# Kernel tuning notes

Measured on AMD Instinct MI355X. Metric: run time of the kernel, lower is better.

## Reference

```python
import jax, jax.numpy as jnp
import numpy as np

B, T, N, H = 512, 128, 256, 256  # batch, time_step, input_size, hidden_size


def setup_inputs() -> dict:
    key = jax.random.key(0)
    ks = jax.random.split(key, 8)
    s_lin = 1.0 / np.sqrt(T)
    s_ih = 1.0 / np.sqrt(H)
    return {
        "X": jax.random.normal(ks[0], (B, T, N), dtype=jnp.float32),
        "Wq": jax.random.uniform(ks[1], (T, T), jnp.float32, -s_lin, s_lin),
        "Wk": jax.random.uniform(ks[2], (T, T), jnp.float32, -s_lin, s_lin),
        "Wv": jax.random.uniform(ks[3], (T, T), jnp.float32, -s_lin, s_lin),
        "W_ih": jax.random.uniform(ks[4], (4 * H, N), jnp.float32, -s_ih, s_ih),
        "W_hh": jax.random.uniform(ks[5], (4 * H, H), jnp.float32, -s_ih, s_ih),
        "b_ih": jax.random.uniform(ks[6], (4 * H,), jnp.float32, -s_ih, s_ih),
        "b_hh": jax.random.uniform(ks[7], (4 * H,), jnp.float32, -s_ih, s_ih),
    }


def _forward(X, Wq, Wk, Wv, W_ih, W_hh, b_ih, b_hh):
    b, t, n = X.shape
    Xp = jnp.swapaxes(X, 1, 2)  # (B, N, T)
    Q = Xp @ Wq.T               # (B, N, T)
    K = Xp @ Wk.T               # (B, N, T)
    V = Xp @ Wv.T               # (B, N, T)
    # QK[b,i,j] = sum_t Q[b,i,t] * K[b,j,t]; scale by sqrt(N)
    scores = jnp.einsum('bit,bjt->bij', Q, K) / jnp.sqrt(jnp.float32(n))
    A = jax.nn.softmax(scores, axis=-1)          # (B, N, N)
    Xa = jnp.einsum('bij,bjt->bit', A, V)        # (B, N, T)
    Xa = jnp.swapaxes(Xa, 1, 2)                  # (B, T, N)

    h0 = jnp.zeros((b, W_hh.shape[1]), X.dtype)
    c0 = h0

    def step(carry, x_t):
        h, c = carry
        gates = x_t @ W_ih.T + b_ih + h @ W_hh.T + b_hh  # (B, 4H)
        i, f, g, o = jnp.split(gates, 4, axis=-1)         # PyTorch gate order
        i = jax.nn.sigmoid(i)
        f = jax.nn.sigmoid(f)
        g = jnp.tanh(g)
        o = jax.nn.sigmoid(o)
        c = f * c + i * g
        h = o * jnp.tanh(c)
        return (h, c), h

    _, hs = jax.lax.scan(step, (h0, c0), jnp.swapaxes(Xa, 0, 1))  # (T, B, H)
    return jnp.swapaxes(hs, 0, 1)  # (B, T, H)


def reference(X, Wq, Wk, Wv, W_ih, W_hh, b_ih, b_hh):
    return _forward(X, Wq, Wk, Wv, W_ih, W_hh, b_ih, b_hh)
```

## Files before the change

### kernel.cpp

```cpp
#include <hip/hip_runtime.h>
#include <hip/hip_bf16.h>
#include <stdint.h>


#define DI __device__ __forceinline__

typedef __attribute__((ext_vector_type(8))) short bf16x8;
typedef __attribute__((ext_vector_type(4))) short short4v;
typedef __attribute__((ext_vector_type(4))) float f32x4;
typedef __attribute__((ext_vector_type(4))) int int4v;

union U8 { bf16x8 v; short4v h[2]; int4v i; };

DI unsigned short f2bf(float x){
  union { float f; unsigned u; } v; v.f = x;
  unsigned r = v.u + 0x7fffu + ((v.u >> 16) & 1u);
  return (unsigned short)(r >> 16);
}
DI float bf2f(unsigned short x){
  union { unsigned u; float f; } v; v.u = ((unsigned)x) << 16; return v.f;
}
DI float rcp_(float x){ return __builtin_amdgcn_rcpf(x); }
DI float sigm(float x){ return rcp_(1.0f + __expf(-x)); }
DI float tanhf_(float x){ return 1.0f - 2.0f * rcp_(1.0f + __expf(2.0f * x)); }

#define BB 512
#define TT 128
#define NN 256
#define HH 256

__global__ void k_prep(const float* __restrict__ Wq, const float* __restrict__ Wk,
                       const float* __restrict__ Wv, const float* __restrict__ Wih,
                       const float* __restrict__ bih, const float* __restrict__ bhh,
                       unsigned short* __restrict__ wqb, unsigned short* __restrict__ wkb,
                       unsigned short* __restrict__ wvb, unsigned short* __restrict__ wihb,
                       float* __restrict__ bias, int* __restrict__ flags){
  int i = blockIdx.x * 256 + threadIdx.x;
  if (i < 16384){ wqb[i] = f2bf(Wq[i]); wkb[i] = f2bf(Wk[i]); wvb[i] = f2bf(Wv[i]); }
  if (i < 262144){ wihb[i] = f2bf(Wih[i]); }
  if (i < 1024){ bias[i] = bih[i] + bhh[i]; }
  if (i < 256){ flags[i] = 0; }
}

__global__ void k_prep2(const float* __restrict__ Whh, unsigned short* __restrict__ whh_f){
  int idx = blockIdx.x * 256 + threadIdx.x;
  int j = idx >> 3, kk = idx & 7;
  const float* src = Whh + j * 256 + kk * 32;
  unsigned short o[32];
  #pragma unroll
  for (int g = 0; g < 4; ++g)
    #pragma unroll
    for (int e = 0; e < 4; ++e){
      o[g * 8 + e]     = f2bf(src[4 * g + e]);
      o[g * 8 + 4 + e] = f2bf(src[16 + 4 * g + e]);
    }
  int4v* dst = (int4v*)((char*)whh_f + j * 512 + kk * 64);
  #pragma unroll
  for (int q = 0; q < 4; ++q) dst[q] = *(int4v*)(o + q * 8);
}

__global__ __launch_bounds__(256) void k_xpose(const float* __restrict__ X,
                                               unsigned short* __restrict__ Xp){
  __shared__ float tile[128][65];
  int b = blockIdx.y, n0 = blockIdx.x * 64;
  int tid = threadIdx.x;
  int nloc = tid & 63, t0 = tid >> 6;
  const float* src = X + (size_t)b * TT * NN + n0 + nloc;
  #pragma unroll
  for (int r = 0; r < 32; ++r){
    int t = r * 4 + t0;
    tile[t][nloc] = src[(size_t)t * NN];
  }
  __syncthreads();
  int tl = tid & 127, nr0 = tid >> 7;
  unsigned short* dst = Xp + ((size_t)b * NN + n0) * TT + tl;
  #pragma unroll
  for (int r = 0; r < 32; ++r){
    int n = r * 2 + nr0;
    dst[(size_t)n * TT] = f2bf(tile[tl][n]);
  }
}

__global__ __launch_bounds__(256) void k_qkv(const unsigned short* __restrict__ Xp,
      const unsigned short* __restrict__ Wqb, const unsigned short* __restrict__ Wkb,
      const unsigned short* __restrict__ Wvb,
      unsigned short* __restrict__ Qo, unsigned short* __restrict__ Ko,
      unsigned short* __restrict__ Vo){
  __shared__ __align__(16) char smem[32768 + 8192];
  unsigned short* Bs = (unsigned short*)smem;
  char* As = smem + 32768;
  char* Os = smem;
  int mode = blockIdx.y;
  const unsigned short* W = (mode == 0) ? Wqb : ((mode == 1) ? Wkb : Wvb);
  int m0 = blockIdx.x * 128;
  int tid = threadIdx.x;

  #pragma unroll
  for (int it = 0; it < 16; ++it){
    int c = it * 256 + tid;
    int j = c >> 5;
    int kc = (c & 31) << 2;
    short4v v = *(const short4v*)(W + j * 128 + kc);
    *(short4v*)((char*)Bs + j * 256 + ((kc * 2) ^ ((j & 7) << 4))) = v;
  }

  int lane = tid & 63, wv = tid >> 6;
  int wr = wv >> 1, wc = wv & 1;
  int l15 = lane & 15, g = lane >> 4;
  f32x4 zro = {0.f, 0.f, 0.f, 0.f};
  f32x4 acc[4][4];
  #pragma unroll
  for (int a = 0; a < 4; ++a)
    #pragma unroll
    for (int bq = 0; bq < 4; ++bq) acc[a][bq] = zro;

  int arow = tid >> 1, ahalf = (tid & 1) * 16;
  const unsigned short* Ap = Xp + (size_t)(m0 + arow) * 128;

  for (int ks = 0; ks < 4; ++ks){
    __syncthreads();
    {
      const unsigned short* s = Ap + ks * 32 + ahalf;
      char* base = As + arow * 64;
      int kb = ahalf * 2;
      int sw = (arow & 7) << 3;
      *(short4v*)(base + ((kb     ) ^ sw)) = *(const short4v*)(s);
      *(short4v*)(base + ((kb +  8) ^ sw)) = *(const short4v*)(s + 4);
      *(short4v*)(base + ((kb + 16) ^ sw)) = *(const short4v*)(s + 8);
      *(short4v*)(base + ((kb + 24) ^ sw)) = *(const short4v*)(s + 12);
    }
    __syncthreads();
    U8 af[4];
    #pragma unroll
    for (int mt = 0; mt < 4; ++mt){
      int ar = wr * 64 + mt * 16 + l15;
      const char* ab = As + ar * 64;
      int sw = (ar & 7) << 3;
      af[mt].h[0] = *(const short4v*)(ab + ((8 * g) ^ sw));
      af[mt].h[1] = *(const short4v*)(ab + ((8 * g + 32) ^ sw));
    }
    #pragma unroll
    for (int nt = 0; nt < 4; ++nt){
      int jr = wc * 64 + nt * 16 + l15;
      const char* bb = (const char*)Bs + jr * 256;
      int kb = ks * 64 + 8 * g, sw = (jr & 7) << 4;
      U8 bf;
      bf.h[0] = *(const short4v*)(bb + (kb ^ sw));
      bf.h[1] = *(const short4v*)(bb + ((kb + 32) ^ sw));
      #pragma unroll
      for (int mt = 0; mt < 4; ++mt)
        acc[mt][nt] = __builtin_amdgcn_mfma_f32_16x16x32_bf16(af[mt].v, bf.v, acc[mt][nt], 0, 0, 0);
    }
  }
  __syncthreads();
  float scale = (mode == 0) ? 0.0625f : 1.0f;
  #pragma unroll
  for (int mt = 0; mt < 4; ++mt)
    #pragma unroll
    for (int nt = 0; nt < 4; ++nt)
      #pragma unroll
      for (int r = 0; r < 4; ++r){
        int row = wr * 64 + mt * 16 + g * 4 + r;
        int col = wc * 64 + nt * 16 + l15;
        unsigned short hv = f2bf(acc[mt][nt][r] * scale);
        int addr = (mode == 2) ? (col * 256 + ((row * 2) ^ ((col & 7) << 4)))
                               : (row * 256 + ((col * 2) ^ ((row & 7) << 4)));
        *(unsigned short*)(Os + addr) = hv;
      }
  __syncthreads();
  int orow = tid >> 1, oseg = tid & 1;
  const char* srcrow = Os + orow * 256;
  unsigned short* dst;
  if (mode == 2){
    int bq = m0 >> 8, ibase = m0 & 255;
    dst = Vo + ((size_t)bq * 128 + orow) * 256 + ibase + oseg * 64;
  } else {
    dst = ((mode == 0) ? Qo : Ko) + (size_t)(m0 + orow) * 128 + oseg * 64;
  }
  #pragma unroll
  for (int c = 0; c < 8; ++c){
    int kb = oseg * 128 + c * 16;
    *(int4v*)((char*)dst + c * 16) = *(const int4v*)(srcrow + (kb ^ ((orow & 7) << 4)));
  }
}

__global__ __launch_bounds__(256) void k_attn(const unsigned short* __restrict__ Q,
        const unsigned short* __restrict__ K, const unsigned short* __restrict__ Vt,
        unsigned short* __restrict__ Xa){
  __shared__ __align__(16) char smem[16384 + 65536 + 32768 + 256];
  char* Qs = smem;
  char* Ks = smem + 16384;
  char* Ps = smem + 16384 + 65536;
  float* rden = (float*)(smem + 16384 + 65536 + 32768);
  int b = blockIdx.y, i0 = blockIdx.x * 64;
  int tid = threadIdx.x, lane = tid & 63, wv = tid >> 6;
  int l15 = lane & 15, g = lane >> 4;

  {
    int row = tid >> 2, q = tid & 3;
    const char* src = (const char*)(Q + ((size_t)b * 256 + i0 + row) * 128) + q * 64;
    char* dstr = Qs + row * 256;
    int sw = (row & 7) << 4;
    #pragma unroll
    for (int c = 0; c < 4; ++c){
      int kb = q * 64 + c * 16;
      *(int4v*)(dstr + (kb ^ sw)) = *(const int4v*)(src + c * 16);
    }
  }
  {
    const char* src = (const char*)(K + ((size_t)b * 256 + tid) * 128);
    char* dstr = Ks + tid * 256;
    int sw = (tid & 7) << 4;
    #pragma unroll
    for (int c = 0; c < 16; ++c)
      *(int4v*)(dstr + ((c * 16) ^ sw)) = *(const int4v*)(src + c * 16);
  }
  __syncthreads();

  f32x4 zro = {0.f, 0.f, 0.f, 0.f};
  f32x4 acc[16];
  #pragma unroll
  for (int nt = 0; nt < 16; ++nt) acc[nt] = zro;
  #pragma unroll
  for (int kk = 0; kk < 4; ++kk){
    int ar = wv * 16 + l15;
    const char* ab = Qs + ar * 256;
    int kb = kk * 64 + 8 * g, swa = (ar & 7) << 4;
    U8 a;
    a.h[0] = *(const short4v*)(ab + (kb ^ swa));
    a.h[1] = *(const short4v*)(ab + ((kb + 32) ^ swa));
    #pragma unroll
    for (int nt = 0; nt < 16; ++nt){
      int jr = nt * 16 + l15;
      const char* bb = Ks + jr * 256;
      int swb = (jr & 7) << 4;
      U8 bf;
      bf.h[0] = *(const short4v*)(bb + (kb ^ swb));
      bf.h[1] = *(const short4v*)(bb + ((kb + 32) ^ swb));
      acc[nt] = __builtin_amdgcn_mfma_f32_16x16x32_bf16(a.v, bf.v, acc[nt], 0, 0, 0);
    }
  }
  float mx[4], sm[4];
  #pragma unroll
  for (int r = 0; r < 4; ++r){
    float m = acc[0][r];
    #pragma unroll
    for (int nt = 1; nt < 16; ++nt) m = fmaxf(m, acc[nt][r]);
    #pragma unroll
    for (int s = 1; s < 16; s <<= 1) m = fmaxf(m, __shfl_xor(m, s));
    mx[r] = m;
  }
  #pragma unroll
  for (int r = 0; r < 4; ++r){
    float s = 0.f;
    #pragma unroll
    for (int nt = 0; nt < 16; ++nt){
      float p = __expf(acc[nt][r] - mx[r]);
      acc[nt][r] = p; s += p;
    }
    #pragma unroll
    for (int sd = 1; sd < 16; sd <<= 1) s += __shfl_xor(s, sd);
    sm[r] = s;
  }
  #pragma unroll
  for (int nt = 0; nt < 16; ++nt)
    #pragma unroll
    for (int r = 0; r < 4; ++r){
      int ir = wv * 16 + g * 4 + r;
      *(unsigned short*)(Ps + ir * 512 + ((nt * 16 + l15) * 2 ^ ((ir & 7) << 4))) = f2bf(acc[nt][r]);
    }
  #pragma unroll
  for (int r = 0; r < 4; ++r)
    if (l15 == r) rden[wv * 16 + g * 4 + r] = rcp_(sm[r]);
  __syncthreads();
  {
    int row = tid >> 1, half = tid & 1;
    const char* src = (const char*)(Vt + ((size_t)b * 128 + row) * 256) + half * 256;
    char* dstr = Ks + row * 512;
    int sw = (row & 7) << 4;
    #pragma unroll
    for (int c = 0; c < 16; ++c){
      int jb = half * 256 + c * 16;
      *(int4v*)(dstr + (jb ^ sw)) = *(const int4v*)(src + c * 16);
    }
  }
  __syncthreads();

  f32x4 acc2[2][4];
  #pragma unroll
  for (int mt = 0; mt < 2; ++mt)
    #pragma unroll
    for (int nt = 0; nt < 4; ++nt) acc2[mt][nt] = zro;
  #pragma unroll
  for (int kk = 0; kk < 8; ++kk){
    int kb = kk * 64 + 8 * g;
    U8 bfr[4];
    #pragma unroll
    for (int nt = 0; nt < 4; ++nt){
      int ir = nt * 16 + l15;
      const char* pb = Ps + ir * 512;
      int sw = (ir & 7) << 4;
      bfr[nt].h[0] = *(const short4v*)(pb + (kb ^ sw));
      bfr[nt].h[1] = *(const short4v*)(pb + ((kb + 32) ^ sw));
    }
    #pragma unroll
    for (int mt = 0; mt < 2; ++mt){
      int tr = wv * 32 + mt * 16 + l15;
      const char* ab = Ks + tr * 512;
      int sw = (tr & 7) << 4;
      U8 a;
      a.h[0] = *(const short4v*)(ab + (kb ^ sw));
      a.h[1] = *(const short4v*)(ab + ((kb + 32) ^ sw));
      #pragma unroll
      for (int nt = 0; nt < 4; ++nt)
        acc2[mt][nt] = __builtin_amdgcn_mfma_f32_16x16x32_bf16(a.v, bfr[nt].v, acc2[mt][nt], 0, 0, 0);
    }
  }
  #pragma unroll
  for (int nt = 0; nt < 4; ++nt){
    float rd = rden[nt * 16 + l15];
    #pragma unroll
    for (int mt = 0; mt < 2; ++mt)
      #pragma unroll
      for (int r = 0; r < 4; ++r){
        int t = wv * 32 + mt * 16 + g * 4 + r;
        int i = i0 + nt * 16 + l15;
        Xa[((size_t)b * 128 + t) * 256 + i] = f2bf(acc2[mt][nt][r] * rd);
      }
  }
}

template<bool WXF32>
__global__ __launch_bounds__(256) void k_wx(const unsigned short* __restrict__ Xa,
        const unsigned short* __restrict__ Wih, const float* __restrict__ bias,
        void* __restrict__ WxT){
  __shared__ __align__(16) char smem[65536 + 8192];
  char* Bsm = smem;
  char* As = smem + 65536;
  int bidx = blockIdx.x;
  int j0 = blockIdx.y * 128;
  int tid = threadIdx.x;
  {
    int row = tid >> 1, half = tid & 1;
    const char* src = (const char*)(Wih + (size_t)(j0 + row) * 256) + half * 256;
    char* dstr = Bsm + row * 512;
    int sw = (row & 7) << 4;
    #pragma unroll
    for (int c = 0; c < 16; ++c){
      int kb = half * 256 + c * 16;
      *(int4v*)(dstr + (kb ^ sw)) = *(const int4v*)(src + c * 16);
    }
  }
  int lane = tid & 63, wv = tid >> 6, wr = wv >> 1, wc = wv & 1;
  int l15 = lane & 15, g = lane >> 4;
  f32x4 zro = {0.f, 0.f, 0.f, 0.f};
  f32x4 acc[4][4];
  #pragma unroll
  for (int a = 0; a < 4; ++a)
    #pragma unroll
    for (int bq = 0; bq < 4; ++bq) acc[a][bq] = zro;
  int arow = tid >> 1, ahalf = (tid & 1) * 16;
  const unsigned short* Ap = Xa + (size_t)(bidx * 128 + arow) * 256;
  for (int ks = 0; ks < 8; ++ks){
    __syncthreads();
    {
      const unsigned short* s = Ap + ks * 32 + ahalf;
      char* base = As + arow * 64;
      int kb = ahalf * 2, sw = (arow & 7) << 3;
      *(short4v*)(base + ((kb     ) ^ sw)) = *(const short4v*)(s);
      *(short4v*)(base + ((kb +  8) ^ sw)) = *(const short4v*)(s + 4);
      *(short4v*)(base + ((kb + 16) ^ sw)) = *(const short4v*)(s + 8);
      *(short4v*)(base + ((kb + 24) ^ sw)) = *(const short4v*)(s + 12);
    }
    __syncthreads();
    U8 af[4];
    #pragma unroll
    for (int mt = 0; mt < 4; ++mt){
      int ar = wr * 64 + mt * 16 + l15;
      const char* ab = As + ar * 64;
      int sw = (ar & 7) << 3;
      af[mt].h[0] = *(const short4v*)(ab + ((8 * g) ^ sw));
      af[mt].h[1] = *(const short4v*)(ab + ((8 * g + 32) ^ sw));
    }
    #pragma unroll
    for (int nt = 0; nt < 4; ++nt){
      int jr = wc * 64 + nt * 16 + l15;
      const char* bb = Bsm + jr * 512;
      int kb = ks * 64 + 8 * g, sw = (jr & 7) << 4;
      U8 bf;
      bf.h[0] = *(const short4v*)(bb + (kb ^ sw));
      bf.h[1] = *(const short4v*)(bb + ((kb + 32) ^ sw));
      #pragma unroll
      for (int mt = 0; mt < 4; ++mt)
        acc[mt][nt] = __builtin_amdgcn_mfma_f32_16x16x32_bf16(af[mt].v, bf.v, acc[mt][nt], 0, 0, 0);
    }
  }
  #pragma unroll
  for (int nt = 0; nt < 4; ++nt){
    int j = j0 + wc * 64 + nt * 16 + l15;
    float bs = bias[j];
    #pragma unroll
    for (int mt = 0; mt < 4; ++mt)
      #pragma unroll
      for (int r = 0; r < 4; ++r){
        int t = wr * 64 + mt * 16 + g * 4 + r;
        float v = acc[mt][nt][r] + bs;
        size_t o = ((size_t)t * 512 + bidx) * 1024 + j;
        if (WXF32) ((float*)WxT)[o] = v;
        else       ((unsigned short*)WxT)[o] = f2bf(v);
      }
  }
}

template<bool WXF32>
__global__ __launch_bounds__(512, 2) void k_lstm5(const void* __restrict__ WxT,
        const unsigned short* __restrict__ whh_f, float* __restrict__ out,
        unsigned int* __restrict__ hbuf, int* __restrict__ flags){
  __shared__ __align__(16) char smem[8192 + 8448];
  char* HS = smem;
  float* GS = (float*)(smem + 8192);
  int tid = threadIdx.x, lane = tid & 63, wv = tid >> 6;
  int l15 = lane & 15, g = lane >> 4;
  int bid = blockIdx.x;
  int x = bid & 7, q = bid >> 3;
  int y = q >> 2, m = q & 3;
  int grp = y * 8 + x;
  int b0 = grp * 8;
  int c0 = m * 64;
  int tb = tid >> 6, tc = tid & 63;

  U8 breg[2][8];
  #pragma unroll
  for (int nt = 0; nt < 2; ++nt){
    int jl = wv * 32 + nt * 16 + l15;
    int jg = (jl >> 6) * 256 + c0 + (jl & 63);
    #pragma unroll
    for (int kk = 0; kk < 8; ++kk)
      breg[nt][kk].i = *(const int4v*)((const char*)whh_f + (size_t)jg * 512 + kk * 64 + g * 16);
  }
  { int4v z = {0,0,0,0}; *(int4v*)(HS + tid * 16) = z; }
  float cst = 0.f;
  __syncthreads();

  float wx[4];
  {
    size_t ob = ((size_t)b0 + tb) * 1024 + c0 + tc;
    #pragma unroll
    for (int gate = 0; gate < 4; ++gate)
      wx[gate] = WXF32 ? ((const float*)WxT)[ob + gate * 256]
                       : bf2f(((const unsigned short*)WxT)[ob + gate * 256]);
  }

  int swA = (l15 & 7) << 3;
  const char* hsrow = HS + l15 * 512;
  int keep = g >> 1;
  #pragma unroll 1
  for (int t = 0; t < 128; ++t){
    f32x4 zro = {0.f, 0.f, 0.f, 0.f};
    f32x4 acc[2] = {zro, zro};
    #pragma unroll
    for (int kk = 0; kk < 8; ++kk){
      U8 a;
      a.h[0] = *(const short4v*)(hsrow + ((kk * 64 + 8 * g) ^ swA));
      a.h[1] = *(const short4v*)(hsrow + ((kk * 64 + 32 + 8 * g) ^ swA));
      acc[0] = __builtin_amdgcn_mfma_f32_16x16x32_bf16(a.v, breg[0][kk].v, acc[0], 0, 0, 0);
      acc[1] = __builtin_amdgcn_mfma_f32_16x16x32_bf16(a.v, breg[1][kk].v, acc[1], 0, 0, 0);
    }
    #pragma unroll
    for (int r = 0; r < 4; ++r){
      float v0 = acc[0][r], v1 = acc[1][r];
      float kv = keep ? v1 : v0;
      float sv = keep ? v0 : v1;
      float val = kv + __shfl_xor(sv, 32);
      int jl = wv * 32 + keep * 16 + l15;
      int batch = (g & 1) * 4 + r;
      GS[batch * 264 + (jl >> 6) * 66 + (jl & 63)] = val;
    }
    __syncthreads();
    float gv0 = GS[tb * 264 +   0 + tc];
    float gv1 = GS[tb * 264 +  66 + tc];
    float gv2 = GS[tb * 264 + 132 + tc];
    float gv3 = GS[tb * 264 + 198 + tc];
    float wxn[4] = {0.f, 0.f, 0.f, 0.f};
    if (t < 127){
      size_t ob = ((size_t)(t + 1) * 512 + b0 + tb) * 1024 + c0 + tc;
      #pragma unroll
      for (int gate = 0; gate < 4; ++gate)
        wxn[gate] = WXF32 ? ((const float*)WxT)[ob + gate * 256]
                          : bf2f(((const unsigned short*)WxT)[ob + gate * 256]);
    }
    float gi = sigm(gv0 + wx[0]);
    float gf = sigm(gv1 + wx[1]);
    float gg = tanhf_(gv2 + wx[2]);
    float go = sigm(gv3 + wx[3]);
    float c = gf * cst + gi * gg;
    cst = c;
    float h = go * tanhf_(c);
    out[((size_t)(b0 + tb) * 128 + t) * 256 + c0 + tc] = h;
    if (t < 127){
      unsigned short hhi = f2bf(h);
      unsigned short hlo = f2bf(h - bf2f(hhi));
      unsigned int pk = (unsigned int)hhi | ((unsigned int)hlo << 16);
      unsigned int* hb = hbuf + ((size_t)grp * 2 + (t & 1)) * 2048;
      __hip_atomic_store(hb + tb * 256 + c0 + tc, pk, __ATOMIC_RELAXED, __HIP_MEMORY_SCOPE_SYSTEM);
      __syncthreads();
      if (wv == 0){
        if (lane == 0)
          __hip_atomic_store(&flags[grp * 4 + m], t + 1, __ATOMIC_RELAXED, __HIP_MEMORY_SCOPE_SYSTEM);
        if (lane >= 1 && lane <= 3){
          int pl = lane - 1;
          int pslot = pl + (pl >= m ? 1 : 0);
          while (__hip_atomic_load(&flags[grp * 4 + pslot], __ATOMIC_RELAXED,
                                   __HIP_MEMORY_SCOPE_SYSTEM) <= t){}
        }
      }
      __syncthreads();
      {
        int bb = tid >> 6, cg = tid & 63;
        const unsigned long long* sp =
            (const unsigned long long*)(hb + bb * 256 + cg * 4);
        unsigned long long w0 = __hip_atomic_load(sp,     __ATOMIC_RELAXED, __HIP_MEMORY_SCOPE_SYSTEM);
        unsigned long long w1 = __hip_atomic_load(sp + 1, __ATOMIC_RELAXED, __HIP_MEMORY_SCOPE_SYSTEM);
        unsigned int u0 = (unsigned int)w0, u1 = (unsigned int)(w0 >> 32);
        unsigned int u2 = (unsigned int)w1, u3 = (unsigned int)(w1 >> 32);
        short4v hiv = { (short)(u0 & 0xffff), (short)(u1 & 0xffff),
                        (short)(u2 & 0xffff), (short)(u3 & 0xffff) };
        short4v lov = { (short)(u0 >> 16), (short)(u1 >> 16),
                        (short)(u2 >> 16), (short)(u3 >> 16) };
        int sw = (bb & 7) << 3;
        int cb = (cg * 8) ^ sw;
        *(short4v*)(HS + bb * 512 + cb) = hiv;
        *(short4v*)(HS + (bb + 8) * 512 + cb) = lov;
      }
      __syncthreads();
      wx[0] = wxn[0]; wx[1] = wxn[1]; wx[2] = wxn[2]; wx[3] = wxn[3];
    }
  }
}

extern "C" void kernel_launch(void* const* d_in, const int* in_sizes, int n_in,
                              void* d_out, int out_size, void* d_ws, size_t ws_size,
                              hipStream_t stream){
  (void)in_sizes; (void)n_in; (void)out_size;
  const float* X   = (const float*)d_in[0];
  const float* Wq  = (const float*)d_in[1];
  const float* Wk  = (const float*)d_in[2];
  const float* Wv  = (const float*)d_in[3];
  const float* Wih = (const float*)d_in[4];
  const float* Whh = (const float*)d_in[5];
  const float* bih = (const float*)d_in[6];
  const float* bhh = (const float*)d_in[7];
  float* out = (float*)d_out;
  char* ws = (char*)d_ws;

  const size_t SZ  = 33554432ULL;
  const size_t WXF = 268435456ULL;
  const size_t WTS = 2200000ULL;
  bool wxf32 = ws_size >= WXF + SZ + WTS;
  size_t wxb = wxf32 ? WXF : WXF / 2;

  unsigned short* p_xp = (unsigned short*)ws;
  unsigned short* p_q  = (unsigned short*)(ws + SZ);
  unsigned short* p_k  = (unsigned short*)(ws + 2 * SZ);
  unsigned short* p_vt = (unsigned short*)(ws + 3 * SZ);
  void* p_wx = (void*)ws;
  char* p = ws + wxb;
  unsigned short* p_xa  = (unsigned short*)p; p += SZ;
  unsigned short* p_wqb = (unsigned short*)p; p += 32768;
  unsigned short* p_wkb = (unsigned short*)p; p += 32768;
  unsigned short* p_wvb = (unsigned short*)p; p += 32768;
  unsigned short* p_wihb= (unsigned short*)p; p += 524288;
  unsigned short* p_whhf= (unsigned short*)p; p += 524288;
  float* p_bias = (float*)p; p += 4096;
  unsigned int* p_hbuf = (unsigned int*)p; p += 1048576;
  int* p_flags = (int*)p;

  k_prep<<<1024, 256, 0, stream>>>(Wq, Wk, Wv, Wih, bih, bhh,
                                   p_wqb, p_wkb, p_wvb, p_wihb, p_bias, p_flags);
  k_prep2<<<32, 256, 0, stream>>>(Whh, p_whhf);
  k_xpose<<<dim3(4, 512), 256, 0, stream>>>(X, p_xp);
  k_qkv<<<dim3(1024, 3), 256, 0, stream>>>(p_xp, p_wqb, p_wkb, p_wvb, p_q, p_k, p_vt);
  k_attn<<<dim3(4, 512), 256, 0, stream>>>(p_q, p_k, p_vt, p_xa);
  if (wxf32){
    k_wx<true><<<dim3(512, 8), 256, 0, stream>>>(p_xa, p_wihb, p_bias, p_wx);
    k_lstm5<true><<<256, 512, 0, stream>>>(p_wx, p_whhf, out, p_hbuf, p_flags);
  } else {
    k_wx<false><<<dim3(512, 8), 256, 0, stream>>>(p_xa, p_wihb, p_bias, p_wx);
    k_lstm5<false><<<256, 512, 0, stream>>>(p_wx, p_whhf, out, p_hbuf, p_flags);
  }
}
```

Measured before the change: 613.6 us.

## Replace flag-based cross-block barrier with sequence-tagged hidden-state polling

After: 750.4 us. 22.3% more time.

```diff
diff --git a/kernel.cpp b/kernel.cpp
--- a/kernel.cpp
+++ b/kernel.cpp
@@ -34,12 +34,11 @@
                        const float* __restrict__ bih, const float* __restrict__ bhh,
                        unsigned short* __restrict__ wqb, unsigned short* __restrict__ wkb,
                        unsigned short* __restrict__ wvb, unsigned short* __restrict__ wihb,
-                       float* __restrict__ bias, int* __restrict__ flags){
+                       float* __restrict__ bias, unsigned long long* __restrict__ hbuf){
   int i = blockIdx.x * 256 + threadIdx.x;
   if (i < 16384){ wqb[i] = f2bf(Wq[i]); wkb[i] = f2bf(Wk[i]); wvb[i] = f2bf(Wv[i]); }
-  if (i < 262144){ wihb[i] = f2bf(Wih[i]); }
+  if (i < 262144){ wihb[i] = f2bf(Wih[i]); hbuf[i] = 0ULL; }
   if (i < 1024){ bias[i] = bih[i] + bhh[i]; }
-  if (i < 256){ flags[i] = 0; }
 }
 
 __global__ void k_prep2(const float* __restrict__ Whh, unsigned short* __restrict__ whh_f){
@@ -413,9 +412,9 @@
 }
 
 template<bool WXF32>
-__global__ __launch_bounds__(512, 2) void k_lstm5(const void* __restrict__ WxT,
+__global__ __launch_bounds__(512, 2) void k_lstm6(const void* __restrict__ WxT,
         const unsigned short* __restrict__ whh_f, float* __restrict__ out,
-        unsigned int* __restrict__ hbuf, int* __restrict__ flags){
+        unsigned long long* __restrict__ hbuf){
   __shared__ __align__(16) char smem[8192 + 8448];
   char* HS = smem;
   float* GS = (float*)(smem + 8192);
@@ -501,28 +500,26 @@
       unsigned short hhi = f2bf(h);
       unsigned short hlo = f2bf(h - bf2f(hhi));
       unsigned int pk = (unsigned int)hhi | ((unsigned int)hlo << 16);
-      unsigned int* hb = hbuf + ((size_t)grp * 2 + (t & 1)) * 2048;
-      __hip_atomic_store(hb + tb * 256 + c0 + tc, pk, __ATOMIC_RELAXED, __HIP_MEMORY_SCOPE_SYSTEM);
-      __syncthreads();
-      if (wv == 0){
-        if (lane == 0)
-          __hip_atomic_store(&flags[grp * 4 + m], t + 1, __ATOMIC_RELAXED, __HIP_MEMORY_SCOPE_SYSTEM);
-        if (lane >= 1 && lane <= 3){
-          int pl = lane - 1;
-          int pslot = pl + (pl >= m ? 1 : 0);
-          while (__hip_atomic_load(&flags[grp * 4 + pslot], __ATOMIC_RELAXED,
-                                   __HIP_MEMORY_SCOPE_SYSTEM) <= t){}
-        }
-      }
-      __syncthreads();
+      unsigned long long* hb = hbuf + ((size_t)grp * 2 + (t & 1)) * 2048;
+      __hip_atomic_store(hb + tb * 256 + c0 + tc,
+                         ((unsigned long long)(t + 1) << 32) | (unsigned long long)pk,
+                         __ATOMIC_RELAXED, __HIP_MEMORY_SCOPE_SYSTEM);
       {
         int bb = tid >> 6, cg = tid & 63;
-        const unsigned long long* sp =
-            (const unsigned long long*)(hb + bb * 256 + cg * 4);
-        unsigned long long w0 = __hip_atomic_load(sp,     __ATOMIC_RELAXED, __HIP_MEMORY_SCOPE_SYSTEM);
-        unsigned long long w1 = __hip_atomic_load(sp + 1, __ATOMIC_RELAXED, __HIP_MEMORY_SCOPE_SYSTEM);
-        unsigned int u0 = (unsigned int)w0, u1 = (unsigned int)(w0 >> 32);
-        unsigned int u2 = (unsigned int)w1, u3 = (unsigned int)(w1 >> 32);
+        unsigned long long* sp = hb + bb * 256 + cg * 4;
+        unsigned long long w0, w1, w2, w3;
+        unsigned int want = (unsigned int)(t + 1);
+        for (int it = 0; it < (1 << 27); ++it){
+          w0 = __hip_atomic_load(sp,     __ATOMIC_RELAXED, __HIP_MEMORY_SCOPE_SYSTEM);
+          w1 = __hip_atomic_load(sp + 1, __ATOMIC_RELAXED, __HIP_MEMORY_SCOPE_SYSTEM);
+          w2 = __hip_atomic_load(sp + 2, __ATOMIC_RELAXED, __HIP_MEMORY_SCOPE_SYSTEM);
+          w3 = __hip_atomic_load(sp + 3, __ATOMIC_RELAXED, __HIP_MEMORY_SCOPE_SYSTEM);
+          if ((unsigned int)(w0 >> 32) == want && (unsigned int)(w1 >> 32) == want &&
+              (unsigned int)(w2 >> 32) == want && (unsigned int)(w3 >> 32) == want) break;
+          __builtin_amdgcn_s_sleep(1);
+        }
+        unsigned int u0 = (unsigned int)w0, u1 = (unsigned int)w1;
+        unsigned int u2 = (unsigned int)w2, u3 = (unsigned int)w3;
         short4v hiv = { (short)(u0 & 0xffff), (short)(u1 & 0xffff),
                         (short)(u2 & 0xffff), (short)(u3 & 0xffff) };
         short4v lov = { (short)(u0 >> 16), (short)(u1 >> 16),
@@ -555,7 +552,7 @@
 
   const size_t SZ  = 33554432ULL;
   const size_t WXF = 268435456ULL;
-  const size_t WTS = 2200000ULL;
+  const size_t WTS = 3300000ULL;
   bool wxf32 = ws_size >= WXF + SZ + WTS;
   size_t wxb = wxf32 ? WXF : WXF / 2;
 
@@ -565,27 +562,26 @@
   unsigned short* p_vt = (unsigned short*)(ws + 3 * SZ);
   void* p_wx = (void*)ws;
   char* p = ws + wxb;
-  unsigned short* p_xa  = (unsigned short*)p; p += SZ;
+  unsigned short* p_xa  = (unsigned short*)p; p += 33554432;
   unsigned short* p_wqb = (unsigned short*)p; p += 32768;
   unsigned short* p_wkb = (unsigned short*)p; p += 32768;
   unsigned short* p_wvb = (unsigned short*)p; p += 32768;
   unsigned short* p_wihb= (unsigned short*)p; p += 524288;
   unsigned short* p_whhf= (unsigned short*)p; p += 524288;
   float* p_bias = (float*)p; p += 4096;
-  unsigned int* p_hbuf = (unsigned int*)p; p += 1048576;
-  int* p_flags = (int*)p;
+  unsigned long long* p_hbuf = (unsigned long long*)p;
 
   k_prep<<<1024, 256, 0, stream>>>(Wq, Wk, Wv, Wih, bih, bhh,
-                                   p_wqb, p_wkb, p_wvb, p_wihb, p_bias, p_flags);
+                                   p_wqb, p_wkb, p_wvb, p_wihb, p_bias, p_hbuf);
   k_prep2<<<32, 256, 0, stream>>>(Whh, p_whhf);
   k_xpose<<<dim3(4, 512), 256, 0, stream>>>(X, p_xp);
   k_qkv<<<dim3(1024, 3), 256, 0, stream>>>(p_xp, p_wqb, p_wkb, p_wvb, p_q, p_k, p_vt);
   k_attn<<<dim3(4, 512), 256, 0, stream>>>(p_q, p_k, p_vt, p_xa);
   if (wxf32){
     k_wx<true><<<dim3(512, 8), 256, 0, stream>>>(p_xa, p_wihb, p_bias, p_wx);
-    k_lstm5<true><<<256, 512, 0, stream>>>(p_wx, p_whhf, out, p_hbuf, p_flags);
+    k_lstm6<true><<<256, 512, 0, stream>>>(p_wx, p_whhf, out, p_hbuf);
   } else {
     k_wx<false><<<dim3(512, 8), 256, 0, stream>>>(p_xa, p_wihb, p_bias, p_wx);
-    k_lstm5<false><<<256, 512, 0, stream>>>(p_wx, p_whhf, out, p_hbuf, p_flags);
-  }
-}
+    k_lstm6<false><<<256, 512, 0, stream>>>(p_wx, p_whhf, out, p_hbuf);
+  }
+}
```
